# Performance work log

Measured on AMD Instinct MI355X. Metric: run time of the kernel, lower is better.

## Reference

```python
import jax, jax.numpy as jnp
import numpy as np

N, F, E = 2048, 4, 65536
D, H, FF = 256, 4, 2048  # d_model, n_heads, transformer feedforward dim
HD = D // H


def setup_inputs() -> dict:
    key = jax.random.key(0)
    ks = jax.random.split(key, 26)
    p = lambda k, shape, fan_in: (jax.random.normal(k, shape, jnp.float32) / np.sqrt(fan_in))
    return {
        "features": jax.random.normal(ks[0], (N, F), jnp.float32),
        "edges": jax.random.randint(ks[1], (2, E), 0, N, jnp.int64),
        # Embedder.linear: Linear(1, 256)
        "lin_w": p(ks[2], (D, 1), 1), "lin_b": jnp.zeros((D,), jnp.float32),
        # TransformerEncoderLayer self-attention
        "in_proj_w": p(ks[3], (3 * D, D), D), "in_proj_b": jnp.zeros((3 * D,), jnp.float32),
        "out_w": p(ks[4], (D, D), D), "out_b": jnp.zeros((D,), jnp.float32),
        "ln1_g": jnp.ones((D,), jnp.float32), "ln1_b": jnp.zeros((D,), jnp.float32),
        # feedforward
        "ffn_w1": p(ks[5], (FF, D), D), "ffn_b1": jnp.zeros((FF,), jnp.float32),
        "ffn_w2": p(ks[6], (D, FF), FF), "ffn_b2": jnp.zeros((D,), jnp.float32),
        "ln2_g": jnp.ones((D,), jnp.float32), "ln2_b": jnp.zeros((D,), jnp.float32),
        # 4 GCNConv layers (torch Linear convention: weight [out, in])
        "W1": p(ks[7], (512, D), D), "b1": jnp.zeros((512,), jnp.float32),
        "W2": p(ks[8], (512, 512), 512), "b2": jnp.zeros((512,), jnp.float32),
        "W3": p(ks[9], (512, 512), 512), "b3": jnp.zeros((512,), jnp.float32),
        "W4": p(ks[10], (512, 512), 512), "b4": jnp.zeros((512,), jnp.float32),
    }


def _layer_norm(x, g, b, eps=1e-5):
    m = jnp.mean(x, axis=-1, keepdims=True)
    v = jnp.mean((x - m) ** 2, axis=-1, keepdims=True)
    return (x - m) / jnp.sqrt(v + eps) * g + b


def _gcn_conv(x, W, b, src, dst, n):
    # PyG GCNConv: h = x @ W^T; add self-loops; norm = deg^-1/2[src]*deg^-1/2[dst];
    # out = scatter_add(norm * h[src] -> dst) + bias
    h = x @ W.T
    loop = jnp.arange(n, dtype=src.dtype)
    s = jnp.concatenate([src, loop])
    d = jnp.concatenate([dst, loop])
    deg = jax.ops.segment_sum(jnp.ones_like(d, dtype=h.dtype), d, num_segments=n)
    dinv = jnp.where(deg > 0, deg ** -0.5, 0.0)
    norm = dinv[s] * dinv[d]
    return jax.ops.segment_sum(h[s] * norm[:, None], d, num_segments=n) + b


def reference(features, edges, lin_w, lin_b, in_proj_w, in_proj_b, out_w, out_b,
              ln1_g, ln1_b, ffn_w1, ffn_b1, ffn_w2, ffn_b2, ln2_g, ln2_b,
              W1, b1, W2, b2, W3, b3, W4, b4):
    n, f = features.shape
    # Embedder: [N,F,1] -> Linear(1,D) -> [N,F,D]; seq-first transformer (seq=N, batch=F)
    x = features[..., None] @ lin_w.T + lin_b  # [N,F,D]
    qkv = x @ in_proj_w.T + in_proj_b          # [N,F,3D]
    q, k, v = jnp.split(qkv, 3, axis=-1)
    split = lambda t: t.reshape(n, f, H, HD).transpose(1, 2, 0, 3)  # [F,H,N,hd]
    q, k, v = split(q), split(k), split(v)
    scores = jnp.einsum('bhqd,bhkd->bhqk', q, k) / np.sqrt(HD)      # [F,H,N,N]
    attn = jax.nn.softmax(scores, axis=-1)
    o = jnp.einsum('bhqk,bhkd->bhqd', attn, v).transpose(2, 0, 1, 3).reshape(n, f, D)
    o = o @ out_w.T + out_b
    x = _layer_norm(x + o, ln1_g, ln1_b)
    ff = jax.nn.relu(x @ ffn_w1.T + ffn_b1) @ ffn_w2.T + ffn_b2
    x = _layer_norm(x + ff, ln2_g, ln2_b)
    x = jax.nn.relu(jnp.mean(x, axis=1))  # mean over feature-batch dim -> [N,D]

    src, dst = edges[0], edges[1]
    x = jax.nn.relu(_gcn_conv(x, W1, b1, src, dst, n))
    x = jax.nn.relu(_gcn_conv(x, W2, b2, src, dst, n))
    x = jax.nn.relu(_gcn_conv(x, W3, b3, src, dst, n))
    x = _gcn_conv(x, W4, b4, src, dst, n)
    return x
```

## Files before the change

kernel.cpp:

```cpp
#include <hip/hip_runtime.h>
#include <hip/hip_bf16.h>
#include <math.h>

#define NN   2048
#define FB   4
#define DD   256
#define EE   65536
#define NT   (NN*FB)
#define FFD  2048

typedef unsigned int u32;
typedef unsigned short u16;
typedef __attribute__((ext_vector_type(4))) float f32x4;
typedef __attribute__((ext_vector_type(8))) short bf16x8;

#define OFF_W2   0
#define OFF_G1   524288
#define OFF_G2   655360
#define OFF_G3   917504
#define OFF_G4   1179648
#define WBF_TOT  1441792

__device__ float g_A[768], g_B[768];
__device__ float g_coefA[4], g_coefC[4];
__device__ float g_meanv[6], g_G[36];
__device__ float g_Vx[8*DD];
__device__ u16   g_w1vh[FFD*8];
__device__ float g_m[NT*4];
__device__ float g_cc[NT*8];
__device__ u16   g_xmh[NN*DD];
__device__ u16   g_hsh[NN*512];
__device__ u16   g_xgh[NN*512];
__device__ u16   g_wbf[WBF_TOT];
__device__ __align__(64) int g_degp[NN*16];
__device__ __align__(64) int g_curp[NN*16];
__device__ int   g_off[NN+1], g_adj[EE];
__device__ float g_dinv[NN];

__device__ __forceinline__ u16 f2bf(float x) {
  u32 u = __float_as_uint(x);
  return (u16)((u + 0x7FFFu + ((u >> 16) & 1u)) >> 16);
}
__device__ __forceinline__ float bfl(u32 v) { return __uint_as_float(v << 16); }
__device__ __forceinline__ float bfh(u32 v) { return __uint_as_float(v & 0xffff0000u); }
__device__ __forceinline__ void gl_lds16(const void* g, void* l) {
  __builtin_amdgcn_global_load_lds(
      (const __attribute__((address_space(1))) u32*)g,
      (__attribute__((address_space(3))) u32*)l, 16, 0, 0);
}
__device__ __forceinline__ float qred(float v) {
  v += __shfl_xor(v, 1, 64);
  v += __shfl_xor(v, 2, 64);
  return v;
}
__device__ __forceinline__ void acc8(const uint4 v, float* a) {
  a[0]+=bfl(v.x); a[1]+=bfh(v.x);
  a[2]+=bfl(v.y); a[3]+=bfh(v.y);
  a[4]+=bfl(v.z); a[5]+=bfh(v.z);
  a[6]+=bfl(v.w); a[7]+=bfh(v.w);
}

__global__ __launch_bounds__(256) void k_fuse1(const float* __restrict__ ipw,
    const float* __restrict__ ipb, const float* __restrict__ linw,
    const float* __restrict__ linb) {
  __shared__ __align__(16) float sm[512];
  const int b = blockIdx.x, t = threadIdx.x;
  if (b < 12) {
    float* lw = sm; float* lb = sm + 256;
    lw[t] = linw[t]; lb[t] = linb[t];
    __syncthreads();
    int j = b*64 + (t>>2), c = t&3;
    const float4* row = (const float4*)&ipw[j*256 + c*64];
    float a = 0.f, bb = 0.f;
    #pragma unroll
    for (int q = 0; q < 16; q++) {
      float4 v = row[q]; int d0 = c*64 + q*4;
      a  += v.x*lw[d0] + v.y*lw[d0+1] + v.z*lw[d0+2] + v.w*lw[d0+3];
      bb += v.x*lb[d0] + v.y*lb[d0+1] + v.z*lb[d0+2] + v.w*lb[d0+3];
    }
    a = qred(a); bb = qred(bb);
    if (c == 0) { g_A[j] = a; g_B[j] = bb + ipb[j]; }
  } else {
    int i = (b - 12)*256 + t;
    if (i < NN*16) { g_degp[i] = 0; g_curp[i] = 0; }
  }
}

__global__ __launch_bounds__(256) void k_fuse2(const float* __restrict__ outw,
    const float* __restrict__ outb, const float* __restrict__ linw,
    const float* __restrict__ linb, const float* __restrict__ g1,
    const float* __restrict__ b1ln, const int* __restrict__ edges) {
  __shared__ __align__(16) float sm[512 + 4*27];
  const int b = blockIdx.x, t = threadIdx.x;
  if (b == 0) {
    int lane = t & 63, w = t >> 6;
    {
      float aq = g_A[w*64 + lane], ak = g_A[256 + w*64 + lane], bq = g_B[w*64 + lane];
      float pa = aq * ak, pc = bq * ak;
      #pragma unroll
      for (int o = 32; o > 0; o >>= 1) { pa += __shfl_down(pa, o, 64); pc += __shfl_down(pc, o, 64); }
      if (lane == 0) { g_coefA[w] = pa * 0.125f; g_coefC[w] = pc * 0.125f; }
    }
    float* A2 = sm; float* B2 = sm + 256; float* wred = sm + 512;
    A2[t] = g_A[512 + t]; B2[t] = g_B[512 + t];
    __syncthreads();
    const int d = t;
    const float4* row = (const float4*)&outw[d*256];
    float pv[4] = {0,0,0,0}, q0 = 0.f;
    #pragma unroll 8
    for (int q = 0; q < 64; q++) {
      float4 v = row[q]; int e0 = q*4; int h = q >> 4;
      pv[h] += v.x*A2[e0] + v.y*A2[e0+1] + v.z*A2[e0+2] + v.w*A2[e0+3];
      q0    += v.x*B2[e0] + v.y*B2[e0+1] + v.z*B2[e0+2] + v.w*B2[e0+3];
    }
    q0 += outb[d];
    float c0 = linb[d] + q0;
    float Mv[6] = { linw[d], pv[0], pv[1], pv[2], pv[3], c0 };
    float vals[27];
    { int idx = 0;
      #pragma unroll
      for (int k = 0; k < 6; k++) vals[idx++] = Mv[k];
      #pragma unroll
      for (int k = 0; k < 6; k++)
        #pragma unroll
        for (int l = 0; l < 6; l++) if (l >= k) vals[idx++] = Mv[k]*Mv[l];
    }
    #pragma unroll
    for (int k2 = 0; k2 < 27; k2++) {
      float v = vals[k2];
      #pragma unroll
      for (int o = 32; o > 0; o >>= 1) v += __shfl_down(v, o, 64);
      if (lane == 0) wred[w*27 + k2] = v;
    }
    __syncthreads();
    if (t < 27) {
      float s = wred[t] + wred[27 + t] + wred[54 + t] + wred[81 + t];
      if (t < 6) g_meanv[t] = s * (1.f/256.f);
      else {
        int p = t - 6, k = 0;
        while (p >= 6 - k) { p -= 6 - k; k++; }
        int l = k + p;
        g_G[k*6+l] = s; g_G[l*6+k] = s;
      }
    }
    #pragma unroll
    for (int k = 0; k < 6; k++) g_Vx[k*256 + d] = Mv[k] * g1[d];
    g_Vx[6*256 + d] = g1[d];
    g_Vx[7*256 + d] = b1ln[d];
  } else {
    int e = (b - 1)*256 + t;
    atomicAdd(&g_degp[edges[EE + e] * 16], 1);
  }
}

__global__ __launch_bounds__(256) void k_fuse3(const float* __restrict__ feat,
    const float* __restrict__ w1, const float* __restrict__ fb1,
    const float* __restrict__ w2c, const float* __restrict__ W1c,
    const float* __restrict__ W2c, const float* __restrict__ W3c,
    const float* __restrict__ W4c) {
  __shared__ __align__(16) char smraw[34816];
  const int b = blockIdx.x, t = threadIdx.x;
  if (b < 512) {
    float* fs = (float*)smraw;
    float* ss = fs + 8192;
    float* ww = ss + 256;
    for (int i = t; i < 2048; i += 256) {
      const float4 v = *(const float4*)&feat[i*4];
      fs[0*2048+i] = v.x; fs[1*2048+i] = v.y; fs[2*2048+i] = v.z; fs[3*2048+i] = v.w;
    }
    __syncthreads();
    int tuple = b * 64 + (t >> 2);
    int c = t & 3;
    int h = tuple & 3, f = (tuple >> 2) & 3, n = tuple >> 4;
    float fi = fs[f*2048 + n];
    float tt = g_coefA[h] * fi + g_coefC[h];
    float s = 0.f, wsum = 0.f;
    int j0 = c * 512;
    for (int j = j0; j < j0 + 512; j++) {
      float fj = fs[f*2048 + j];
      float e = __expf(tt * fj);
      s += e; wsum += e * fj;
    }
    ss[(t>>2)*4 + c] = s; ww[(t>>2)*4 + c] = wsum;
    __syncthreads();
    if (c == 0) {
      float S = ss[(t>>2)*4] + ss[(t>>2)*4+1] + ss[(t>>2)*4+2] + ss[(t>>2)*4+3];
      float W = ww[(t>>2)*4] + ww[(t>>2)*4+1] + ww[(t>>2)*4+2] + ww[(t>>2)*4+3];
      g_m[tuple] = W / S;
    }
  } else if (b < 544) {
    float* vx = (float*)smraw;
    #pragma unroll
    for (int k = 0; k < 8; k++) vx[k*256 + t] = g_Vx[k*256 + t];
    __syncthreads();
    int j = (b - 512)*64 + (t>>2), c = t&3;
    const float4* row = (const float4*)&w1[j*256 + c*64];
    float acc[8] = {0,0,0,0,0,0,0,0};
    #pragma unroll
    for (int q = 0; q < 16; q++) {
      float4 v = row[q]; int d0 = c*64 + q*4;
      #pragma unroll
      for (int k = 0; k < 8; k++)
        acc[k] += v.x*vx[k*256+d0] + v.y*vx[k*256+d0+1]
                + v.z*vx[k*256+d0+2] + v.w*vx[k*256+d0+3];
    }
    #pragma unroll
    for (int k = 0; k < 8; k++) acc[k] = qred(acc[k]);
    if (c == 0) {
      acc[7] += fb1[j];
      uint4 r;
      r.x = ((u32)f2bf(acc[1])<<16) | f2bf(acc[0]);
      r.y = ((u32)f2bf(acc[3])<<16) | f2bf(acc[2]);
      r.z = ((u32)f2bf(acc[5])<<16) | f2bf(acc[4]);
      r.w = ((u32)f2bf(acc[7])<<16) | f2bf(acc[6]);
      *(uint4*)&g_w1vh[j*8] = r;
    }
  } else if (b == 544) {
    int* wt = (int*)smraw;
    int base = t * 8;
    int v[8], ex[8], sum = 0;
    #pragma unroll
    for (int i = 0; i < 8; i++) { ex[i] = sum; v[i] = g_degp[(base+i)*16]; sum += v[i]; }
    int lane = t & 63, w = t >> 6;
    int inc = sum;
    #pragma unroll
    for (int o = 1; o < 64; o <<= 1) { int x = __shfl_up(inc, o, 64); if (lane >= o) inc += x; }
    if (lane == 63) wt[w] = inc;
    __syncthreads();
    int wb = 0;
    for (int j = 0; j < w; j++) wb += wt[j];
    int excl = wb + inc - sum;
    #pragma unroll
    for (int i = 0; i < 8; i++) {
      g_off[base+i] = excl + ex[i];
      g_dinv[base+i] = rsqrtf((float)(v[i] + 1));
    }
    if (t == 255) g_off[NN] = wb + inc;
  } else {
    int i = ((b - 545)*256 + t) * 4;
    const float* src; int off;
    if (i < OFF_G1)      { src = w2c; off = OFF_W2; }
    else if (i < OFF_G2) { src = W1c; off = OFF_G1; }
    else if (i < OFF_G3) { src = W2c; off = OFF_G2; }
    else if (i < OFF_G4) { src = W3c; off = OFF_G3; }
    else                 { src = W4c; off = OFF_G4; }
    float4 v = *(const float4*)&src[i - off];
    ushort4 r;
    r.x = f2bf(v.x); r.y = f2bf(v.y); r.z = f2bf(v.z); r.w = f2bf(v.w);
    *(ushort4*)&g_wbf[i] = r;
  }
}

__global__ __launch_bounds__(256) void k_fuse4(const float* __restrict__ feat,
                                               const int* __restrict__ edges) {
  const int b = blockIdx.x, t = threadIdx.x;
  if (b < 32) {
    int tok = b * 256 + t;
    int n = tok >> 2, f = tok & 3;
    float fi = feat[n*4 + f];
    float u[6] = { fi, g_m[tok*4+0], g_m[tok*4+1], g_m[tok*4+2], g_m[tok*4+3], 1.f };
    float mu = 0.f;
    #pragma unroll
    for (int k = 0; k < 6; k++) mu += g_meanv[k] * u[k];
    float q = 0.f;
    for (int k = 0; k < 6; k++)
      for (int l = 0; l < 6; l++) q += u[k] * g_G[k*6+l] * u[l];
    q *= (1.f/256.f);
    float var = q - mu * mu;
    float s = rsqrtf(var + 1e-5f);
    float4 w0; w0.x = fi*s; w0.y = u[1]*s; w0.z = u[2]*s; w0.w = u[3]*s;
    float4 w1v; w1v.x = u[4]*s; w1v.y = s; w1v.z = -mu*s; w1v.w = 1.f;
    *(float4*)&g_cc[tok*8]     = w0;
    *(float4*)&g_cc[tok*8 + 4] = w1v;
  } else {
    int e = (b - 32)*256 + t;
    int s = edges[e], d = edges[EE + e];
    int pos = atomicAdd(&g_curp[d*16], 1);
    g_adj[g_off[d] + pos] = s;
  }
}

__global__ __launch_bounds__(256) void k_ffnln(const float* __restrict__ fb2,
    const float* __restrict__ ln2g, const float* __restrict__ ln2b) {
  __shared__ __align__(16) char smp[50176];
  u16*   Bsl  = (u16*)smp;
  u16*   Asl  = (u16*)(smp + 32768);
  float* ccs  = (float*)(smp + 36864);
  float* vxs  = (float*)(smp + 37888);
  float* fb2s = (float*)(smp + 46080);
  float* g2s  = (float*)(smp + 47104);
  float* b2s  = (float*)(smp + 48128);
  float* part = (float*)(smp + 49152);

  const int b = blockIdx.x, t = threadIdx.x;
  const int w = t >> 6, lane = t & 63, fr = lane & 15, gk = lane >> 4;
  const int tok0 = b * 32;

  for (int i = t; i < 2048; i += 256) vxs[i] = g_Vx[i];
  if (t < 64)              ((float4*)ccs)[t]        = ((const float4*)&g_cc[tok0*8])[t];
  else if (t < 128)        ((float4*)fb2s)[t-64]    = ((const float4*)fb2)[t-64];
  else if (t < 192)        ((float4*)g2s)[t-128]    = ((const float4*)ln2g)[t-128];
  else                     ((float4*)b2s)[t-192]    = ((const float4*)ln2b)[t-192];
  __syncthreads();

  const int arow = t >> 3, asub = t & 7;
  float ac[8];
  #pragma unroll
  for (int k = 0; k < 8; k++) ac[k] = ccs[arow*8 + k];

  f32x4 acc[2][4] = {};
  const u16* W2p = g_wbf + OFF_W2;
  for (int k0 = 0; k0 < FFD; k0 += 64) {
    {
      float h[8];
      #pragma unroll
      for (int e2 = 0; e2 < 8; e2++) {
        int jj = k0 + asub*8 + e2;
        uint4 wv = *(const uint4*)&g_w1vh[jj*8];
        float s = ac[0]*bfl(wv.x) + ac[1]*bfh(wv.x)
                + ac[2]*bfl(wv.y) + ac[3]*bfh(wv.y)
                + ac[4]*bfl(wv.z) + ac[5]*bfh(wv.z)
                + ac[6]*bfl(wv.w) + ac[7]*bfh(wv.w);
        h[e2] = fmaxf(s, 0.f);
      }
      uint4 r;
      r.x = ((u32)f2bf(h[1])<<16) | f2bf(h[0]);
      r.y = ((u32)f2bf(h[3])<<16) | f2bf(h[2]);
      r.z = ((u32)f2bf(h[5])<<16) | f2bf(h[4]);
      r.w = ((u32)f2bf(h[7])<<16) | f2bf(h[6]);
      *(uint4*)&Asl[(arow << 6) + ((asub ^ (arow & 7)) << 3)] = r;
    }
    #pragma unroll
    for (int c = 0; c < 8; c++) {
      int rr = (w << 6) + (c << 3) + (lane >> 3);
      int s2 = lane & 7;
      int ks = ((s2 ^ (rr & 7)) << 3);
      gl_lds16(W2p + (size_t)rr*FFD + k0 + ks, Bsl + (w << 12) + (c << 9));
    }
    __syncthreads();
    bf16x8 af[2][2], bfv[4][2];
    #pragma unroll
    for (int rb = 0; rb < 2; rb++) {
      int row = rb*16 + fr;
      #pragma unroll
      for (int kk = 0; kk < 2; kk++) {
        int q = (kk << 2) + gk;
        af[rb][kk] = *(const bf16x8*)&Asl[(row << 6) + ((q ^ (row & 7)) << 3)];
      }
    }
    #pragma unroll
    for (int nb = 0; nb < 4; nb++) {
      int col = w*64 + nb*16 + fr;
      #pragma unroll
      for (int kk = 0; kk < 2; kk++) {
        int q = (kk << 2) + gk;
        bfv[nb][kk] = *(const bf16x8*)&Bsl[(col << 6) + ((q ^ (col & 7)) << 3)];
      }
    }
    #pragma unroll
    for (int kk = 0; kk < 2; kk++)
      #pragma unroll
      for (int rb = 0; rb < 2; rb++)
        #pragma unroll
        for (int nb = 0; nb < 4; nb++)
          acc[rb][nb] = __builtin_amdgcn_mfma_f32_16x16x32_bf16(af[rb][kk], bfv[nb][kk], acc[rb][nb], 0, 0, 0);
    __syncthreads();
  }

  #pragma unroll
  for (int rb = 0; rb < 2; rb++) {
    #pragma unroll
    for (int nb = 0; nb < 4; nb++) {
      int col = w*64 + nb*16 + fr;
      float fb = fb2s[col];
      #pragma unroll
      for (int r = 0; r < 4; r++) {
        int row = rb*16 + gk*4 + r;
        float x1 = 0.f;
        #pragma unroll
        for (int k = 0; k < 8; k++) x1 += ccs[row*8 + k] * vxs[k*256 + col];
        acc[rb][nb][r] += fb + x1;
      }
    }
  }
  float s1[2][4] = {}, s2v[2][4] = {};
  #pragma unroll
  for (int rb = 0; rb < 2; rb++)
    #pragma unroll
    for (int r = 0; r < 4; r++)
      #pragma unroll
      for (int nb = 0; nb < 4; nb++) {
        float v = acc[rb][nb][r];
        s1[rb][r] += v; s2v[rb][r] += v*v;
      }
  #pragma unroll
  for (int o = 1; o < 16; o <<= 1) {
    #pragma unroll
    for (int rb = 0; rb < 2; rb++)
      #pragma unroll
      for (int r = 0; r < 4; r++) {
        s1[rb][r]  += __shfl_xor(s1[rb][r],  o, 64);
        s2v[rb][r] += __shfl_xor(s2v[rb][r], o, 64);
      }
  }
  if (fr == 0) {
    #pragma unroll
    for (int rb = 0; rb < 2; rb++)
      #pragma unroll
      for (int r = 0; r < 4; r++) {
        int row = rb*16 + gk*4 + r;
        part[(w*32 + row)*2 + 0] = s1[rb][r];
        part[(w*32 + row)*2 + 1] = s2v[rb][r];
      }
  }
  __syncthreads();
  float mu[2][4], inv[2][4];
  #pragma unroll
  for (int rb = 0; rb < 2; rb++)
    #pragma unroll
    for (int r = 0; r < 4; r++) {
      int row = rb*16 + gk*4 + r;
      float S1 = part[row*2] + part[(32+row)*2] + part[(64+row)*2] + part[(96+row)*2];
      float S2 = part[row*2+1] + part[(32+row)*2+1] + part[(64+row)*2+1] + part[(96+row)*2+1];
      float m = S1 * (1.f/256.f);
      mu[rb][r] = m;
      inv[rb][r] = rsqrtf(S2 * (1.f/256.f) - m*m + 1e-5f);
    }
  #pragma unroll
  for (int rb = 0; rb < 2; rb++) {
    int node = b*8 + rb*4 + gk;
    #pragma unroll
    for (int nb = 0; nb < 4; nb++) {
      int col = w*64 + nb*16 + fr;
      float g = g2s[col], bb = b2s[col];
      float m = 0.f;
      #pragma unroll
      for (int r = 0; r < 4; r++)
        m += (acc[rb][nb][r] - mu[rb][r]) * inv[rb][r] * g + bb;
      g_xmh[node*256 + col] = f2bf(fmaxf(m * 0.25f, 0.f));
    }
  }
}

template<int DO_ROWSCALE, int OUT_BF16, int HAS_BIAS>
__global__ __launch_bounds__(256) void k_mm64(
    const u16* __restrict__ A, const u16* __restrict__ Bm, void* __restrict__ Cv,
    int M, int N, int K,
    const float* __restrict__ rowscale, const float* __restrict__ bias)
{
  __shared__ u16 Asl[64*64];
  __shared__ u16 Bsl[64*64];
  const int t = threadIdx.x;
  const int w = t >> 6, lane = t & 63;
  const int bm = blockIdx.y * 64, bn = blockIdx.x * 64;
  const int wr = w >> 1, wc = w & 1;
  const int fr = lane & 15;
  const int gk = lane >> 4;
  const int sslot = lane & 7;
  f32x4 acc[2][2] = {};
  for (int k0 = 0; k0 < K; k0 += 64) {
    #pragma unroll
    for (int c = 0; c < 2; c++) {
      int r = (w << 4) + (c << 3) + (lane >> 3);
      int ks = ((sslot ^ (r & 7)) << 3);
      gl_lds16(A  + (size_t)(bm + r)*K + k0 + ks, Asl + (w << 10) + (c << 9));
      gl_lds16(Bm + (size_t)(bn + r)*K + k0 + ks, Bsl + (w << 10) + (c << 9));
    }
    __syncthreads();
    bf16x8 af[2][2], bfv[2][2];
    #pragma unroll
    for (int rb = 0; rb < 2; rb++) {
      int row = wr*32 + rb*16 + fr;
      #pragma unroll
      for (int kk = 0; kk < 2; kk++) {
        int q = (kk << 2) + gk;
        af[rb][kk] = *(const bf16x8*)&Asl[(row << 6) + ((q ^ (row & 7)) << 3)];
      }
    }
    #pragma unroll
    for (int nb = 0; nb < 2; nb++) {
      int col = wc*32 + nb*16 + fr;
      #pragma unroll
      for (int kk = 0; kk < 2; kk++) {
        int q = (kk << 2) + gk;
        bfv[nb][kk] = *(const bf16x8*)&Bsl[(col << 6) + ((q ^ (col & 7)) << 3)];
      }
    }
    #pragma unroll
    for (int kk = 0; kk < 2; kk++)
      #pragma unroll
      for (int rb = 0; rb < 2; rb++)
        #pragma unroll
        for (int nb = 0; nb < 2; nb++)
          acc[rb][nb] = __builtin_amdgcn_mfma_f32_16x16x32_bf16(af[rb][kk], bfv[nb][kk], acc[rb][nb], 0, 0, 0);
    __syncthreads();
  }
  #pragma unroll
  for (int rb = 0; rb < 2; rb++) {
    #pragma unroll
    for (int r = 0; r < 4; r++) {
      int row = bm + wr*32 + rb*16 + gk*4 + r;
      float rs = DO_ROWSCALE ? rowscale[row] : 1.f;
      #pragma unroll
      for (int nb = 0; nb < 2; nb++) {
        int col = bn + wc*32 + nb*16 + fr;
        float v = acc[rb][nb][r];
        if (HAS_BIAS) v += bias[col];
        if (DO_ROWSCALE) v *= rs;
        if (OUT_BF16) ((u16*)Cv)[(size_t)row*N + col] = f2bf(v);
        else ((float*)Cv)[(size_t)row*N + col] = v;
      }
    }
  }
}

template<int OUT_BF16, int DO_RELU>
__global__ __launch_bounds__(256) void k_agg(const float* __restrict__ bias,
                                             void* __restrict__ outv) {
  const int t = threadIdx.x, w = t >> 6, lane = t & 63;
  const int i = blockIdx.x*4 + w;
  const int d = lane * 8;
  const uint4* tbl = (const uint4*)g_hsh;
  float a[8] = {0,0,0,0,0,0,0,0};
  acc8(tbl[i*64 + lane], a);
  int e0 = g_off[i], e1 = g_off[i+1];
  int e = e0;
  for (; e + 4 <= e1; e += 4) {
    int s0 = g_adj[e+0], s1 = g_adj[e+1], s2 = g_adj[e+2], s3 = g_adj[e+3];
    uint4 v0 = tbl[s0*64 + lane];
    uint4 v1 = tbl[s1*64 + lane];
    uint4 v2 = tbl[s2*64 + lane];
    uint4 v3 = tbl[s3*64 + lane];
    acc8(v0, a); acc8(v1, a); acc8(v2, a); acc8(v3, a);
  }
  for (; e < e1; e++) acc8(tbl[g_adj[e]*64 + lane], a);
  float di = g_dinv[i];
  const float4 b0 = *(const float4*)&bias[d];
  const float4 b1 = *(const float4*)&bias[d+4];
  a[0]=di*a[0]+b0.x; a[1]=di*a[1]+b0.y; a[2]=di*a[2]+b0.z; a[3]=di*a[3]+b0.w;
  a[4]=di*a[4]+b1.x; a[5]=di*a[5]+b1.y; a[6]=di*a[6]+b1.z; a[7]=di*a[7]+b1.w;
  if (DO_RELU) {
    #pragma unroll
    for (int q = 0; q < 8; q++) a[q] = fmaxf(a[q], 0.f);
  }
  if (OUT_BF16) {
    uint4 r;
    r.x = ((u32)f2bf(a[1])<<16) | f2bf(a[0]);
    r.y = ((u32)f2bf(a[3])<<16) | f2bf(a[2]);
    r.z = ((u32)f2bf(a[5])<<16) | f2bf(a[4]);
    r.w = ((u32)f2bf(a[7])<<16) | f2bf(a[6]);
    *(uint4*)&((u16*)outv)[i*512 + d] = r;
  } else {
    float4 r0; r0.x=a[0]; r0.y=a[1]; r0.z=a[2]; r0.w=a[3];
    float4 r1; r1.x=a[4]; r1.y=a[5]; r1.z=a[6]; r1.w=a[7];
    *(float4*)&((float*)outv)[i*512 + d]     = r0;
    *(float4*)&((float*)outv)[i*512 + d + 4] = r1;
  }
}

static float* symf(const void* s) { void* p = nullptr; (void)hipGetSymbolAddress(&p, s); return (float*)p; }

extern "C" void kernel_launch(void* const* d_in, const int* in_sizes, int n_in,
                              void* d_out, int out_size, void* d_ws, size_t ws_size,
                              hipStream_t stream) {
  const float* feat = (const float*)d_in[0];
  const int*   edges= (const int*)  d_in[1];
  const float* linw = (const float*)d_in[2];
  const float* linb = (const float*)d_in[3];
  const float* ipw  = (const float*)d_in[4];
  const float* ipb  = (const float*)d_in[5];
  const float* outw = (const float*)d_in[6];
  const float* outb = (const float*)d_in[7];
  const float* ln1g = (const float*)d_in[8];
  const float* ln1b = (const float*)d_in[9];
  const float* fw1  = (const float*)d_in[10];
  const float* fb1  = (const float*)d_in[11];
  const float* fw2  = (const float*)d_in[12];
  const float* fb2  = (const float*)d_in[13];
  const float* ln2g = (const float*)d_in[14];
  const float* ln2b = (const float*)d_in[15];
  const float* W1g  = (const float*)d_in[16];
  const float* b1g  = (const float*)d_in[17];
  const float* W2g  = (const float*)d_in[18];
  const float* b2g  = (const float*)d_in[19];
  const float* W3g  = (const float*)d_in[20];
  const float* b3g  = (const float*)d_in[21];
  const float* W4g  = (const float*)d_in[22];
  const float* b4g  = (const float*)d_in[23];
  float* out = (float*)d_out;

  u16*   p_xmh = (u16*)symf(HIP_SYMBOL(g_xmh));
  u16*   p_hsh = (u16*)symf(HIP_SYMBOL(g_hsh));
  u16*   p_xgh = (u16*)symf(HIP_SYMBOL(g_xgh));
  u16*   p_wbf = (u16*)symf(HIP_SYMBOL(g_wbf));
  float* p_dinv= symf(HIP_SYMBOL(g_dinv));

  k_fuse1<<<140,  256, 0, stream>>>(ipw, ipb, linw, linb);
  k_fuse2<<<257,  256, 0, stream>>>(outw, outb, linw, linb, ln1g, ln1b, edges);
  k_fuse3<<<1953, 256, 0, stream>>>(feat, fw1, fb1, fw2, W1g, W2g, W3g, W4g);
  k_fuse4<<<288,  256, 0, stream>>>(feat, edges);

  k_ffnln<<<256, 256, 0, stream>>>(fb2, ln2g, ln2b);

  k_mm64<1,1,0><<<dim3(8, 32), 256, 0, stream>>>(
      p_xmh, p_wbf + OFF_G1, p_hsh, NN, 512, 256, p_dinv, nullptr);
  k_agg<1,1><<<NN/4, 256, 0, stream>>>(b1g, p_xgh);
  k_mm64<1,1,0><<<dim3(8, 32), 256, 0, stream>>>(
      p_xgh, p_wbf + OFF_G2, p_hsh, NN, 512, 512, p_dinv, nullptr);
  k_agg<1,1><<<NN/4, 256, 0, stream>>>(b2g, p_xgh);
  k_mm64<1,1,0><<<dim3(8, 32), 256, 0, stream>>>(
      p_xgh, p_wbf + OFF_G3, p_hsh, NN, 512, 512, p_dinv, nullptr);
  k_agg<1,1><<<NN/4, 256, 0, stream>>>(b3g, p_xgh);
  k_mm64<1,1,0><<<dim3(8, 32), 256, 0, stream>>>(
      p_xgh, p_wbf + OFF_G4, p_hsh, NN, 512, 512, p_dinv, nullptr);
  k_agg<0,0><<<NN/4, 256, 0, stream>>>(b4g, out);
}
```

Baseline: 197.2 us.

## Warp-specialize FFN kernel with 512 threads and stage W1 in LDS

```diff
diff --git a/kernel.cpp b/kernel.cpp
--- a/kernel.cpp
+++ b/kernel.cpp
@@ -280,43 +280,53 @@
   }
 }
 
-__global__ __launch_bounds__(256) void k_ffnln(const float* __restrict__ fb2,
+__global__ __launch_bounds__(512) void k_ffnln(const float* __restrict__ fb2,
     const float* __restrict__ ln2g, const float* __restrict__ ln2b) {
-  __shared__ __align__(16) char smp[50176];
+  __shared__ __align__(16) char smp[83968];
   u16*   Bsl  = (u16*)smp;
-  u16*   Asl  = (u16*)(smp + 32768);
-  float* ccs  = (float*)(smp + 36864);
-  float* vxs  = (float*)(smp + 37888);
-  float* fb2s = (float*)(smp + 46080);
-  float* g2s  = (float*)(smp + 47104);
-  float* b2s  = (float*)(smp + 48128);
-  float* part = (float*)(smp + 49152);
+  u16*   w1s  = (u16*)(smp + 32768);
+  u16*   Asl  = (u16*)(smp + 65536);
+  float* ccs  = (float*)(smp + 69632);
+  float* vxs  = (float*)(smp + 70656);
+  float* fb2s = (float*)(smp + 78848);
+  float* g2s  = (float*)(smp + 79872);
+  float* b2s  = (float*)(smp + 80896);
+  float* part = (float*)(smp + 81920);
 
   const int b = blockIdx.x, t = threadIdx.x;
   const int w = t >> 6, lane = t & 63, fr = lane & 15, gk = lane >> 4;
   const int tok0 = b * 32;
 
-  for (int i = t; i < 2048; i += 256) vxs[i] = g_Vx[i];
-  if (t < 64)              ((float4*)ccs)[t]        = ((const float4*)&g_cc[tok0*8])[t];
-  else if (t < 128)        ((float4*)fb2s)[t-64]    = ((const float4*)fb2)[t-64];
-  else if (t < 192)        ((float4*)g2s)[t-128]    = ((const float4*)ln2g)[t-128];
-  else                     ((float4*)b2s)[t-192]    = ((const float4*)ln2b)[t-192];
+  for (int i = t; i < 2048; i += 512) vxs[i] = g_Vx[i];
+  #pragma unroll
+  for (int q = 0; q < 4; q++) {
+    int jj = t + q*512;
+    uint4 v = *(const uint4*)&g_w1vh[jj*8];
+    int idx = (jj & ~7) | ((jj ^ (jj >> 3)) & 7);
+    *(uint4*)&w1s[idx*8] = v;
+  }
+  if (t < 64)          ((float4*)ccs)[t]       = ((const float4*)&g_cc[tok0*8])[t];
+  else if (t < 128)    ((float4*)fb2s)[t-64]   = ((const float4*)fb2)[t-64];
+  else if (t < 192)    ((float4*)g2s)[t-128]   = ((const float4*)ln2g)[t-128];
+  else if (t < 256)    ((float4*)b2s)[t-192]   = ((const float4*)ln2b)[t-192];
   __syncthreads();
 
   const int arow = t >> 3, asub = t & 7;
   float ac[8];
-  #pragma unroll
-  for (int k = 0; k < 8; k++) ac[k] = ccs[arow*8 + k];
-
-  f32x4 acc[2][4] = {};
+  if (t < 256) {
+    #pragma unroll
+    for (int k = 0; k < 8; k++) ac[k] = ccs[arow*8 + k];
+  }
+
+  f32x4 acc[2][2] = {};
   const u16* W2p = g_wbf + OFF_W2;
   for (int k0 = 0; k0 < FFD; k0 += 64) {
-    {
+    if (t < 256) {
       float h[8];
       #pragma unroll
       for (int e2 = 0; e2 < 8; e2++) {
-        int jj = k0 + asub*8 + e2;
-        uint4 wv = *(const uint4*)&g_w1vh[jj*8];
+        int idx = (k0 + 8*asub) | (e2 ^ asub);
+        uint4 wv = *(const uint4*)&w1s[idx*8];
         float s = ac[0]*bfl(wv.x) + ac[1]*bfh(wv.x)
                 + ac[2]*bfl(wv.y) + ac[3]*bfh(wv.y)
                 + ac[4]*bfl(wv.z) + ac[5]*bfh(wv.z)
@@ -329,16 +339,17 @@
       r.z = ((u32)f2bf(h[5])<<16) | f2bf(h[4]);
       r.w = ((u32)f2bf(h[7])<<16) | f2bf(h[6]);
       *(uint4*)&Asl[(arow << 6) + ((asub ^ (arow & 7)) << 3)] = r;
-    }
-    #pragma unroll
-    for (int c = 0; c < 8; c++) {
-      int rr = (w << 6) + (c << 3) + (lane >> 3);
-      int s2 = lane & 7;
-      int ks = ((s2 ^ (rr & 7)) << 3);
-      gl_lds16(W2p + (size_t)rr*FFD + k0 + ks, Bsl + (w << 12) + (c << 9));
-    }
-    __syncthreads();
-    bf16x8 af[2][2], bfv[4][2];
+    } else {
+      const int t2 = t - 256, ws = t2 >> 6, ln = t2 & 63;
+      #pragma unroll
+      for (int c = 0; c < 8; c++) {
+        int rr = (ws << 6) + (c << 3) + (ln >> 3);
+        int ks = (((ln & 7) ^ (rr & 7)) << 3);
+        gl_lds16(W2p + (size_t)rr*FFD + k0 + ks, Bsl + (ws << 12) + (c << 9));
+      }
+    }
+    __syncthreads();
+    bf16x8 af[2][2], bfv[2][2];
     #pragma unroll
     for (int rb = 0; rb < 2; rb++) {
       int row = rb*16 + fr;
@@ -349,8 +360,8 @@
       }
     }
     #pragma unroll
-    for (int nb = 0; nb < 4; nb++) {
-      int col = w*64 + nb*16 + fr;
+    for (int nb = 0; nb < 2; nb++) {
+      int col = w*32 + nb*16 + fr;
       #pragma unroll
       for (int kk = 0; kk < 2; kk++) {
         int q = (kk << 2) + gk;
@@ -362,7 +373,7 @@
       #pragma unroll
       for (int rb = 0; rb < 2; rb++)
         #pragma unroll
-        for (int nb = 0; nb < 4; nb++)
+        for (int nb = 0; nb < 2; nb++)
           acc[rb][nb] = __builtin_amdgcn_mfma_f32_16x16x32_bf16(af[rb][kk], bfv[nb][kk], acc[rb][nb], 0, 0, 0);
     __syncthreads();
   }
@@ -370,8 +381,8 @@
   #pragma unroll
   for (int rb = 0; rb < 2; rb++) {
     #pragma unroll
-    for (int nb = 0; nb < 4; nb++) {
-      int col = w*64 + nb*16 + fr;
+    for (int nb = 0; nb < 2; nb++) {
+      int col = w*32 + nb*16 + fr;
       float fb = fb2s[col];
       #pragma unroll
       for (int r = 0; r < 4; r++) {
@@ -389,7 +400,7 @@
     #pragma unroll
     for (int r = 0; r < 4; r++)
       #pragma unroll
-      for (int nb = 0; nb < 4; nb++) {
+      for (int nb = 0; nb < 2; nb++) {
         float v = acc[rb][nb][r];
         s1[rb][r] += v; s2v[rb][r] += v*v;
       }
@@ -420,8 +431,12 @@
     #pragma unroll
     for (int r = 0; r < 4; r++) {
       int row = rb*16 + gk*4 + r;
-      float S1 = part[row*2] + part[(32+row)*2] + part[(64+row)*2] + part[(96+row)*2];
-      float S2 = part[row*2+1] + part[(32+row)*2+1] + part[(64+row)*2+1] + part[(96+row)*2+1];
+      float S1 = 0.f, S2 = 0.f;
+      #pragma unroll
+      for (int wv = 0; wv < 8; wv++) {
+        S1 += part[(wv*32 + row)*2 + 0];
+        S2 += part[(wv*32 + row)*2 + 1];
+      }
       float m = S1 * (1.f/256.f);
       mu[rb][r] = m;
       inv[rb][r] = rsqrtf(S2 * (1.f/256.f) - m*m + 1e-5f);
@@ -430,8 +445,8 @@
   for (int rb = 0; rb < 2; rb++) {
     int node = b*8 + rb*4 + gk;
     #pragma unroll
-    for (int nb = 0; nb < 4; nb++) {
-      int col = w*64 + nb*16 + fr;
+    for (int nb = 0; nb < 2; nb++) {
+      int col = w*32 + nb*16 + fr;
       float g = g2s[col], bb = b2s[col];
       float m = 0.f;
       #pragma unroll
@@ -600,7 +615,7 @@
   k_fuse3<<<1953, 256, 0, stream>>>(feat, fw1, fb1, fw2, W1g, W2g, W3g, W4g);
   k_fuse4<<<288,  256, 0, stream>>>(feat, edges);
 
-  k_ffnln<<<256, 256, 0, stream>>>(fb2, ln2g, ln2b);
+  k_ffnln<<<256, 512, 0, stream>>>(fb2, ln2g, ln2b);
 
   k_mm64<1,1,0><<<dim3(8, 32), 256, 0, stream>>>(
       p_xmh, p_wbf + OFF_G1, p_hsh, NN, 512, 256, p_dinv, nullptr);
```

Result: faster. 169.3 us (-14.2%).

## Halve row tiles in FFN and GCN GEMMs and stage W1 table in LDS

Applied to the files above, without the earlier changes.

```diff
diff --git a/kernel.cpp b/kernel.cpp
--- a/kernel.cpp
+++ b/kernel.cpp
@@ -282,41 +282,57 @@
 
 __global__ __launch_bounds__(256) void k_ffnln(const float* __restrict__ fb2,
     const float* __restrict__ ln2g, const float* __restrict__ ln2b) {
-  __shared__ __align__(16) char smp[50176];
+  __shared__ __align__(16) char smp[79872];
   u16*   Bsl  = (u16*)smp;
-  u16*   Asl  = (u16*)(smp + 32768);
-  float* ccs  = (float*)(smp + 36864);
-  float* vxs  = (float*)(smp + 37888);
-  float* fb2s = (float*)(smp + 46080);
-  float* g2s  = (float*)(smp + 47104);
-  float* b2s  = (float*)(smp + 48128);
-  float* part = (float*)(smp + 49152);
+  u16*   w1s  = (u16*)(smp + 32768);
+  u16*   Asl  = (u16*)(smp + 65536);
+  float* ccs  = (float*)(smp + 67584);
+  float* vxs  = (float*)(smp + 68096);
+  float* fb2s = (float*)(smp + 76288);
+  float* g2s  = (float*)(smp + 77312);
+  float* b2s  = (float*)(smp + 78336);
+  float* part = (float*)(smp + 79360);
 
   const int b = blockIdx.x, t = threadIdx.x;
   const int w = t >> 6, lane = t & 63, fr = lane & 15, gk = lane >> 4;
-  const int tok0 = b * 32;
+  const int tok0 = b * 16;
 
   for (int i = t; i < 2048; i += 256) vxs[i] = g_Vx[i];
-  if (t < 64)              ((float4*)ccs)[t]        = ((const float4*)&g_cc[tok0*8])[t];
-  else if (t < 128)        ((float4*)fb2s)[t-64]    = ((const float4*)fb2)[t-64];
-  else if (t < 192)        ((float4*)g2s)[t-128]    = ((const float4*)ln2g)[t-128];
-  else                     ((float4*)b2s)[t-192]    = ((const float4*)ln2b)[t-192];
+  #pragma unroll
+  for (int q = 0; q < 8; q++) {
+    int jj = t + q*256;
+    uint4 v = *(const uint4*)&g_w1vh[jj*8];
+    int idx = (jj & ~7) | ((jj ^ (jj >> 3)) & 7);
+    *(uint4*)&w1s[idx*8] = v;
+  }
+  if (t < 32)                     ((float4*)ccs)[t]       = ((const float4*)&g_cc[tok0*8])[t];
+  else if (t >= 64 && t < 128)    ((float4*)fb2s)[t-64]   = ((const float4*)fb2)[t-64];
+  else if (t >= 128 && t < 192)   ((float4*)g2s)[t-128]   = ((const float4*)ln2g)[t-128];
+  else if (t >= 192)              ((float4*)b2s)[t-192]   = ((const float4*)ln2b)[t-192];
   __syncthreads();
 
   const int arow = t >> 3, asub = t & 7;
   float ac[8];
-  #pragma unroll
-  for (int k = 0; k < 8; k++) ac[k] = ccs[arow*8 + k];
-
-  f32x4 acc[2][4] = {};
+  if (t < 128) {
+    #pragma unroll
+    for (int k = 0; k < 8; k++) ac[k] = ccs[arow*8 + k];
+  }
+
+  f32x4 acc[4] = {};
   const u16* W2p = g_wbf + OFF_W2;
   for (int k0 = 0; k0 < FFD; k0 += 64) {
-    {
+    #pragma unroll
+    for (int c = 0; c < 8; c++) {
+      int rr = (w << 6) + (c << 3) + (lane >> 3);
+      int ks = (((lane & 7) ^ (rr & 7)) << 3);
+      gl_lds16(W2p + (size_t)rr*FFD + k0 + ks, Bsl + (w << 12) + (c << 9));
+    }
+    if (t < 128) {
       float h[8];
       #pragma unroll
       for (int e2 = 0; e2 < 8; e2++) {
-        int jj = k0 + asub*8 + e2;
-        uint4 wv = *(const uint4*)&g_w1vh[jj*8];
+        int idx = (k0 + 8*asub) | (e2 ^ asub);
+        uint4 wv = *(const uint4*)&w1s[idx*8];
         float s = ac[0]*bfl(wv.x) + ac[1]*bfh(wv.x)
                 + ac[2]*bfl(wv.y) + ac[3]*bfh(wv.y)
                 + ac[4]*bfl(wv.z) + ac[5]*bfh(wv.z)
@@ -330,23 +346,12 @@
       r.w = ((u32)f2bf(h[7])<<16) | f2bf(h[6]);
       *(uint4*)&Asl[(arow << 6) + ((asub ^ (arow & 7)) << 3)] = r;
     }
-    #pragma unroll
-    for (int c = 0; c < 8; c++) {
-      int rr = (w << 6) + (c << 3) + (lane >> 3);
-      int s2 = lane & 7;
-      int ks = ((s2 ^ (rr & 7)) << 3);
-      gl_lds16(W2p + (size_t)rr*FFD + k0 + ks, Bsl + (w << 12) + (c << 9));
-    }
-    __syncthreads();
-    bf16x8 af[2][2], bfv[4][2];
-    #pragma unroll
-    for (int rb = 0; rb < 2; rb++) {
-      int row = rb*16 + fr;
-      #pragma unroll
-      for (int kk = 0; kk < 2; kk++) {
-        int q = (kk << 2) + gk;
-        af[rb][kk] = *(const bf16x8*)&Asl[(row << 6) + ((q ^ (row & 7)) << 3)];
-      }
+    __syncthreads();
+    bf16x8 af[2], bfv[4][2];
+    #pragma unroll
+    for (int kk = 0; kk < 2; kk++) {
+      int q = (kk << 2) + gk;
+      af[kk] = *(const bf16x8*)&Asl[(fr << 6) + ((q ^ (fr & 7)) << 3)];
     }
     #pragma unroll
     for (int nb = 0; nb < 4; nb++) {
@@ -360,85 +365,73 @@
     #pragma unroll
     for (int kk = 0; kk < 2; kk++)
       #pragma unroll
-      for (int rb = 0; rb < 2; rb++)
-        #pragma unroll
-        for (int nb = 0; nb < 4; nb++)
-          acc[rb][nb] = __builtin_amdgcn_mfma_f32_16x16x32_bf16(af[rb][kk], bfv[nb][kk], acc[rb][nb], 0, 0, 0);
+      for (int nb = 0; nb < 4; nb++)
+        acc[nb] = __builtin_amdgcn_mfma_f32_16x16x32_bf16(af[kk], bfv[nb][kk], acc[nb], 0, 0, 0);
     __syncthreads();
   }
 
   #pragma unroll
-  for (int rb = 0; rb < 2; rb++) {
+  for (int nb = 0; nb < 4; nb++) {
+    int col = w*64 + nb*16 + fr;
+    float fb = fb2s[col];
+    #pragma unroll
+    for (int r = 0; r < 4; r++) {
+      int row = gk*4 + r;
+      float x1 = 0.f;
+      #pragma unroll
+      for (int k = 0; k < 8; k++) x1 += ccs[row*8 + k] * vxs[k*256 + col];
+      acc[nb][r] += fb + x1;
+    }
+  }
+  float s1[4] = {0,0,0,0}, s2v[4] = {0,0,0,0};
+  #pragma unroll
+  for (int r = 0; r < 4; r++)
     #pragma unroll
     for (int nb = 0; nb < 4; nb++) {
-      int col = w*64 + nb*16 + fr;
-      float fb = fb2s[col];
-      #pragma unroll
-      for (int r = 0; r < 4; r++) {
-        int row = rb*16 + gk*4 + r;
-        float x1 = 0.f;
-        #pragma unroll
-        for (int k = 0; k < 8; k++) x1 += ccs[row*8 + k] * vxs[k*256 + col];
-        acc[rb][nb][r] += fb + x1;
-      }
-    }
-  }
-  float s1[2][4] = {}, s2v[2][4] = {};
-  #pragma unroll
-  for (int rb = 0; rb < 2; rb++)
-    #pragma unroll
-    for (int r = 0; r < 4; r++)
-      #pragma unroll
-      for (int nb = 0; nb < 4; nb++) {
-        float v = acc[rb][nb][r];
-        s1[rb][r] += v; s2v[rb][r] += v*v;
-      }
+      float v = acc[nb][r];
+      s1[r] += v; s2v[r] += v*v;
+    }
   #pragma unroll
   for (int o = 1; o < 16; o <<= 1) {
     #pragma unroll
-    for (int rb = 0; rb < 2; rb++)
-      #pragma unroll
-      for (int r = 0; r < 4; r++) {
-        s1[rb][r]  += __shfl_xor(s1[rb][r],  o, 64);
-        s2v[rb][r] += __shfl_xor(s2v[rb][r], o, 64);
-      }
+    for (int r = 0; r < 4; r++) {
+      s1[r]  += __shfl_xor(s1[r],  o, 64);
+      s2v[r] += __shfl_xor(s2v[r], o, 64);
+    }
   }
   if (fr == 0) {
     #pragma unroll
-    for (int rb = 0; rb < 2; rb++)
-      #pragma unroll
-      for (int r = 0; r < 4; r++) {
-        int row = rb*16 + gk*4 + r;
-        part[(w*32 + row)*2 + 0] = s1[rb][r];
-        part[(w*32 + row)*2 + 1] = s2v[rb][r];
-      }
+    for (int r = 0; r < 4; r++) {
+      int row = gk*4 + r;
+      part[(w*16 + row)*2 + 0] = s1[r];
+      part[(w*16 + row)*2 + 1] = s2v[r];
+    }
   }
   __syncthreads();
-  float mu[2][4], inv[2][4];
+  float mu[4], inv[4];
   #pragma unroll
-  for (int rb = 0; rb < 2; rb++)
-    #pragma unroll
-    for (int r = 0; r < 4; r++) {
-      int row = rb*16 + gk*4 + r;
-      float S1 = part[row*2] + part[(32+row)*2] + part[(64+row)*2] + part[(96+row)*2];
-      float S2 = part[row*2+1] + part[(32+row)*2+1] + part[(64+row)*2+1] + part[(96+row)*2+1];
-      float m = S1 * (1.f/256.f);
-      mu[rb][r] = m;
-      inv[rb][r] = rsqrtf(S2 * (1.f/256.f) - m*m + 1e-5f);
-    }
+  for (int r = 0; r < 4; r++) {
+    int row = gk*4 + r;
+    float S1 = 0.f, S2 = 0.f;
+    #pragma unroll
+    for (int wv = 0; wv < 4; wv++) {
+      S1 += part[(wv*16 + row)*2 + 0];
+      S2 += part[(wv*16 + row)*2 + 1];
+    }
+    float m = S1 * (1.f/256.f);
+    mu[r] = m;
+    inv[r] = rsqrtf(S2 * (1.f/256.f) - m*m + 1e-5f);
+  }
+  const int node = b*4 + gk;
   #pragma unroll
-  for (int rb = 0; rb < 2; rb++) {
-    int node = b*8 + rb*4 + gk;
-    #pragma unroll
-    for (int nb = 0; nb < 4; nb++) {
-      int col = w*64 + nb*16 + fr;
-      float g = g2s[col], bb = b2s[col];
-      float m = 0.f;
-      #pragma unroll
-      for (int r = 0; r < 4; r++)
-        m += (acc[rb][nb][r] - mu[rb][r]) * inv[rb][r] * g + bb;
-      g_xmh[node*256 + col] = f2bf(fmaxf(m * 0.25f, 0.f));
-    }
+  for (int nb = 0; nb < 4; nb++) {
+    int col = w*64 + nb*16 + fr;
+    float g = g2s[col], bb = b2s[col];
+    float m = 0.f;
+    #pragma unroll
+    for (int r = 0; r < 4; r++)
+      m += (acc[nb][r] - mu[r]) * inv[r] * g + bb;
+    g_xmh[node*256 + col] = f2bf(fmaxf(m * 0.25f, 0.f));
   }
 }
 
@@ -448,34 +441,34 @@
     int M, int N, int K,
     const float* __restrict__ rowscale, const float* __restrict__ bias)
 {
-  __shared__ u16 Asl[64*64];
+  __shared__ u16 Asl[32*64];
   __shared__ u16 Bsl[64*64];
   const int t = threadIdx.x;
   const int w = t >> 6, lane = t & 63;
-  const int bm = blockIdx.y * 64, bn = blockIdx.x * 64;
+  const int bm = blockIdx.y * 32, bn = blockIdx.x * 64;
   const int wr = w >> 1, wc = w & 1;
   const int fr = lane & 15;
   const int gk = lane >> 4;
-  const int sslot = lane & 7;
-  f32x4 acc[2][2] = {};
+  f32x4 acc[2] = {};
   for (int k0 = 0; k0 < K; k0 += 64) {
+    {
+      int r = (w << 3) + (lane >> 3);
+      int ks = (((lane & 7) ^ (r & 7)) << 3);
+      gl_lds16(A + (size_t)(bm + r)*K + k0 + ks, Asl + (w << 9));
+    }
     #pragma unroll
     for (int c = 0; c < 2; c++) {
-      int r = (w << 4) + (c << 3) + (lane >> 3);
-      int ks = ((sslot ^ (r & 7)) << 3);
-      gl_lds16(A  + (size_t)(bm + r)*K + k0 + ks, Asl + (w << 10) + (c << 9));
-      gl_lds16(Bm + (size_t)(bn + r)*K + k0 + ks, Bsl + (w << 10) + (c << 9));
-    }
-    __syncthreads();
-    bf16x8 af[2][2], bfv[2][2];
-    #pragma unroll
-    for (int rb = 0; rb < 2; rb++) {
-      int row = wr*32 + rb*16 + fr;
-      #pragma unroll
-      for (int kk = 0; kk < 2; kk++) {
-        int q = (kk << 2) + gk;
-        af[rb][kk] = *(const bf16x8*)&Asl[(row << 6) + ((q ^ (row & 7)) << 3)];
-      }
+      int r2 = (w << 4) + (c << 3) + (lane >> 3);
+      int ks2 = (((lane & 7) ^ (r2 & 7)) << 3);
+      gl_lds16(Bm + (size_t)(bn + r2)*K + k0 + ks2, Bsl + (w << 10) + (c << 9));
+    }
+    __syncthreads();
+    bf16x8 af[2], bfv[2][2];
+    #pragma unroll
+    for (int kk = 0; kk < 2; kk++) {
+      int q = (kk << 2) + gk;
+      int row = wr*16 + fr;
+      af[kk] = *(const bf16x8*)&Asl[(row << 6) + ((q ^ (row & 7)) << 3)];
     }
     #pragma unroll
     for (int nb = 0; nb < 2; nb++) {
@@ -489,27 +482,22 @@
     #pragma unroll
     for (int kk = 0; kk < 2; kk++)
       #pragma unroll
-      for (int rb = 0; rb < 2; rb++)
-        #pragma unroll
-        for (int nb = 0; nb < 2; nb++)
-          acc[rb][nb] = __builtin_amdgcn_mfma_f32_16x16x32_bf16(af[rb][kk], bfv[nb][kk], acc[rb][nb], 0, 0, 0);
+      for (int nb = 0; nb < 2; nb++)
+        acc[nb] = __builtin_amdgcn_mfma_f32_16x16x32_bf16(af[kk], bfv[nb][kk], acc[nb], 0, 0, 0);
     __syncthreads();
   }
   #pragma unroll
-  for (int rb = 0; rb < 2; rb++) {
-    #pragma unroll
-    for (int r = 0; r < 4; r++) {
-      int row = bm + wr*32 + rb*16 + gk*4 + r;
-      float rs = DO_ROWSCALE ? rowscale[row] : 1.f;
-      #pragma unroll
-      for (int nb = 0; nb < 2; nb++) {
-        int col = bn + wc*32 + nb*16 + fr;
-        float v = acc[rb][nb][r];
-        if (HAS_BIAS) v += bias[col];
-        if (DO_ROWSCALE) v *= rs;
-        if (OUT_BF16) ((u16*)Cv)[(size_t)row*N + col] = f2bf(v);
-        else ((float*)Cv)[(size_t)row*N + col] = v;
-      }
+  for (int r = 0; r < 4; r++) {
+    int row = bm + wr*16 + gk*4 + r;
+    float rs = DO_ROWSCALE ? rowscale[row] : 1.f;
+    #pragma unroll
+    for (int nb = 0; nb < 2; nb++) {
+      int col = bn + wc*32 + nb*16 + fr;
+      float v = acc[nb][r];
+      if (HAS_BIAS) v += bias[col];
+      if (DO_ROWSCALE) v *= rs;
+      if (OUT_BF16) ((u16*)Cv)[(size_t)row*N + col] = f2bf(v);
+      else ((float*)Cv)[(size_t)row*N + col] = v;
     }
   }
 }
@@ -600,18 +588,18 @@
   k_fuse3<<<1953, 256, 0, stream>>>(feat, fw1, fb1, fw2, W1g, W2g, W3g, W4g);
   k_fuse4<<<288,  256, 0, stream>>>(feat, edges);
 
-  k_ffnln<<<256, 256, 0, stream>>>(fb2, ln2g, ln2b);
-
-  k_mm64<1,1,0><<<dim3(8, 32), 256, 0, stream>>>(
+  k_ffnln<<<512, 256, 0, stream>>>(fb2, ln2g, ln2b);
+
+  k_mm64<1,1,0><<<dim3(8, 64), 256, 0, stream>>>(
       p_xmh, p_wbf + OFF_G1, p_hsh, NN, 512, 256, p_dinv, nullptr);
   k_agg<1,1><<<NN/4, 256, 0, stream>>>(b1g, p_xgh);
-  k_mm64<1,1,0><<<dim3(8, 32), 256, 0, stream>>>(
+  k_mm64<1,1,0><<<dim3(8, 64), 256, 0, stream>>>(
       p_xgh, p_wbf + OFF_G2, p_hsh, NN, 512, 512, p_dinv, nullptr);
   k_agg<1,1><<<NN/4, 256, 0, stream>>>(b2g, p_xgh);
-  k_mm64<1,1,0><<<dim3(8, 32), 256, 0, stream>>>(
+  k_mm64<1,1,0><<<dim3(8, 64), 256, 0, stream>>>(
       p_xgh, p_wbf + OFF_G3, p_hsh, NN, 512, 512, p_dinv, nullptr);
   k_agg<1,1><<<NN/4, 256, 0, stream>>>(b3g, p_xgh);
-  k_mm64<1,1,0><<<dim3(8, 32), 256, 0, stream>>>(
+  k_mm64<1,1,0><<<dim3(8, 64), 256, 0, stream>>>(
       p_xgh, p_wbf + OFF_G4, p_hsh, NN, 512, 512, p_dinv, nullptr);
   k_agg<0,0><<<NN/4, 256, 0, stream>>>(b4g, out);
 }
```

Result: faster. 180.3 us (-8.6%).
